# Optimization experiments

Measured on AMD Instinct MI355X. Metric: run time of the kernel, lower is better.

Reference implementation:

```python
import jax, jax.numpy as jnp
import numpy as np

NUM_EMBEDDINGS = 8192
EMBEDDING_DIM = 512
COMMITMENT_COST = 0.25
EMA_DECAY = 0.99
EPS = 1e-5


def setup_inputs() -> dict:
    key = jax.random.key(0)
    k1, k2, k3, k4 = jax.random.split(key, 4)
    B = 32768
    z = jax.random.normal(k1, (B, EMBEDDING_DIM), dtype=jnp.float32)
    weight = jax.random.normal(k2, (NUM_EMBEDDINGS, EMBEDDING_DIM), dtype=jnp.float32)
    ema_cluster_size = jax.random.uniform(k3, (NUM_EMBEDDINGS,), dtype=jnp.float32)
    ema_dw = jax.random.normal(k4, (NUM_EMBEDDINGS, EMBEDDING_DIM), dtype=jnp.float32)
    return {"z": z, "weight": weight, "ema_cluster_size": ema_cluster_size, "ema_dw": ema_dw}


def reference(z, weight, ema_cluster_size, ema_dw):
    K = weight.shape[0]
    # Squared-L2 distances: (B, K) = |z|^2 + |e|^2 - 2 z e^T
    distances = (
        jnp.sum(z * z, axis=1, keepdims=True)
        + jnp.sum(weight * weight, axis=1)
        - 2.0 * (z @ weight.T)
    )
    indices = jnp.argmin(distances, axis=1)          # (B,)
    quantized_raw = weight[indices]                  # (B, D) gather

    # EMA codebook update (training-mode buffers; one-hot scatter-add == segment_sum)
    counts = jax.ops.segment_sum(jnp.ones(z.shape[0], dtype=z.dtype), indices, num_segments=K)
    dw = jax.ops.segment_sum(z, indices, num_segments=K)  # encodings.T @ z
    new_cluster_size = ema_cluster_size * EMA_DECAY + (1.0 - EMA_DECAY) * counts
    new_ema_dw = ema_dw * EMA_DECAY + (1.0 - EMA_DECAY) * dw
    n = jnp.sum(new_cluster_size)
    cluster_size = (new_cluster_size + EPS) / (n + K * EPS) * n
    new_weight = new_ema_dw / cluster_size[:, None]

    commitment_loss = COMMITMENT_COST * jnp.mean((z - jax.lax.stop_gradient(quantized_raw)) ** 2)
    quantized = z + jax.lax.stop_gradient(quantized_raw - z)  # straight-through
    return quantized, indices, commitment_loss, new_weight, new_cluster_size, new_ema_dw
```

## Files before the change

kernel.cpp:

```cpp
#include <hip/hip_runtime.h>

#define B_N 32768
#define D_N 512
#define K_N 8192
#define EMA 0.99f
#define ONE_M_EMA 0.01f
#define EPS_ 1e-5f
#define CCOST 0.25f

#define ZP_OFF 295936ull
#define WP_OFF 67404800ull
#define WS_NEED (WP_OFF + 16777216ull)
#define CNT_OFF    295936ull
#define OFFS_OFF   332800ull
#define CURS_OFF   365568ull
#define ROWL_OFF   398336ull
#define LPART_OFF  529408ull

typedef __attribute__((ext_vector_type(8))) short bf16x8;
typedef __attribute__((ext_vector_type(4))) float f32x4;

__global__ __launch_bounds__(256) void prep_kernel(const float* __restrict__ w,
                                                   const float* __restrict__ ecs,
                                                   float* __restrict__ wsq,
                                                   float* __restrict__ ncs_out) {
  int row  = blockIdx.x * 4 + (threadIdx.x >> 6);
  int lane = threadIdx.x & 63;
  const float* p = w + (size_t)row * D_N + lane * 8;
  float4 a = *(const float4*)p;
  float4 b = *(const float4*)(p + 4);
  float s = a.x*a.x + a.y*a.y + a.z*a.z + a.w*a.w
          + b.x*b.x + b.y*b.y + b.z*b.z + b.w*b.w;
  #pragma unroll
  for (int off = 32; off; off >>= 1) s += __shfl_down(s, off);
  if (lane == 0) wsq[row] = s;

  int gid = blockIdx.x * 256 + threadIdx.x;
  if (gid < K_N) ncs_out[gid] = EMA * ecs[gid];
}

__global__ __launch_bounds__(256) void prep_nedw(const float4* __restrict__ edw,
                                                 float4* __restrict__ nedw) {
  int i = blockIdx.x * 256 + threadIdx.x;
  float4 v = edw[i];
  v.x *= EMA; v.y *= EMA; v.z *= EMA; v.w *= EMA;
  nedw[i] = v;
}

__global__ __launch_bounds__(256) void split_z(const float* __restrict__ x,
                                               ushort* __restrict__ xp) {
  int g   = blockIdx.x * 256 + threadIdx.x;
  int row = g >> 6, c = g & 63;
  const float* src = x + (size_t)row * 512 + c * 8;
  float v[8];
  *(float4*)&v[0] = *(const float4*)&src[0];
  *(float4*)&v[4] = *(const float4*)&src[4];
  uint hw[4], lw[4];
  #pragma unroll
  for (int i = 0; i < 4; i++) {
    uint b0 = __float_as_uint(v[2*i]);
    uint b1 = __float_as_uint(v[2*i+1]);
    float r0 = v[2*i]   - __uint_as_float(b0 & 0xFFFF0000u);
    float r1 = v[2*i+1] - __uint_as_float(b1 & 0xFFFF0000u);
    hw[i] = (b0 >> 16) | (b1 & 0xFFFF0000u);
    lw[i] = (__float_as_uint(r0) >> 16) | (__float_as_uint(r1) & 0xFFFF0000u);
  }
  int si  = c >> 2;
  int p   = (c & 3) ^ ((row >> 1) & 3);
  size_t sstr = (size_t)B_N * 32;
  size_t base = (size_t)row * 32 + (size_t)p * 8;
  *(uint4*)&xp[(size_t)si * sstr + base]        = (uint4){hw[0], hw[1], hw[2], hw[3]};
  *(uint4*)&xp[(size_t)(16 + si) * sstr + base] = (uint4){lw[0], lw[1], lw[2], lw[3]};
}

__global__ __launch_bounds__(256) void split_w(const float* __restrict__ x,
                                               ushort* __restrict__ xp,
                                               float* __restrict__ wsq) {
  int g   = blockIdx.x * 256 + threadIdx.x;
  int row = g >> 6, c = g & 63;
  const float* src = x + (size_t)row * 512 + c * 8;
  float v[8];
  *(float4*)&v[0] = *(const float4*)&src[0];
  *(float4*)&v[4] = *(const float4*)&src[4];
  uint hw[4], lw[4]; float w2 = 0.f;
  #pragma unroll
  for (int i = 0; i < 4; i++) {
    uint b0 = __float_as_uint(v[2*i]);
    uint b1 = __float_as_uint(v[2*i+1]);
    float r0 = v[2*i]   - __uint_as_float(b0 & 0xFFFF0000u);
    float r1 = v[2*i+1] - __uint_as_float(b1 & 0xFFFF0000u);
    hw[i] = (b0 >> 16) | (b1 & 0xFFFF0000u);
    lw[i] = (__float_as_uint(r0) >> 16) | (__float_as_uint(r1) & 0xFFFF0000u);
    w2 += v[2*i]*v[2*i] + v[2*i+1]*v[2*i+1];
  }
  int si  = c >> 2;
  int p   = (c & 3) ^ ((row >> 1) & 3);
  size_t sstr = (size_t)K_N * 32;
  size_t base = (size_t)row * 32 + (size_t)p * 8;
  *(uint4*)&xp[(size_t)si * sstr + base]        = (uint4){hw[0], hw[1], hw[2], hw[3]};
  *(uint4*)&xp[(size_t)(16 + si) * sstr + base] = (uint4){lw[0], lw[1], lw[2], lw[3]};
  #pragma unroll
  for (int off = 32; off; off >>= 1) w2 += __shfl_down(w2, off);
  if (c == 0) wsq[row] = w2;
}

constexpr int COLT2 = 8;

#define GLDS(SRC, DST) __builtin_amdgcn_global_load_lds((const unsigned int*)(SRC), (unsigned int*)(DST), 16, 0, 0)

#define STAGE4(SS)                                                             \
  {                                                                            \
    const int zsl_ = (sf < 32) ? (sf & 15) : (sf - 16);        \
    const int wsl_ = (sf < 32) ? sf : (sf - 32);               \
    GLDS(zA + (size_t)zsl_ * 2097152,        (char*)As[SS] + t * 16);          \
    GLDS(zA + (size_t)zsl_ * 2097152 + 4096, (char*)As[SS] + 4096 + t * 16);   \
    const size_t wOfs_ = (size_t)wsl_ * 524288 + (size_t)ctf * 16384;          \
    GLDS(wB + wOfs_,         (char*)Bs[SS] + t * 16);                          \
    GLDS(wB + wOfs_ + 4096,  (char*)Bs[SS] + 4096  + t * 16);                  \
    GLDS(wB + wOfs_ + 8192,  (char*)Bs[SS] + 8192  + t * 16);                  \
    GLDS(wB + wOfs_ + 12288, (char*)Bs[SS] + 12288 + t * 16);                  \
    sf++; if (sf == 48) { sf = 0; ctf++; }                                     \
  }

#define LOADFRAG4(AX, BX, RS)                                                  \
  {                                                                            \
    const char* Ab_ = (const char*)As[RS] + aoff;                              \
    const char* Bb_ = (const char*)Bs[RS] + boff;                              \
    _Pragma("unroll")                                                          \
    for (int i_ = 0; i_ < 8; i_++) AX[i_] = *(const bf16x8*)(Ab_ + i_ * 1024); \
    _Pragma("unroll")                                                          \
    for (int j_ = 0; j_ < 4; j_++) BX[j_] = *(const bf16x8*)(Bb_ + j_ * 1024); \
  }

#define MFMABLK4(AX, BX)                                                       \
  {                                                                            \
    __builtin_amdgcn_s_setprio(1);                                             \
    _Pragma("unroll")                                                          \
    for (int i_ = 0; i_ < 8; i_++)                                             \
      _Pragma("unroll")                                                        \
      for (int j_ = 0; j_ < 4; j_++)                                           \
        acc[i_][j_] = __builtin_amdgcn_mfma_f32_16x16x32_bf16(AX[i_], BX[j_],  \
                                                        acc[i_][j_], 0, 0, 0); \
    __builtin_amdgcn_s_setprio(0);                                             \
  }

#define PH4(AC, BC, AL, BL, RS, SS, G)                                         \
  {                                                                            \
    const int g_ = (G);                                                        \
    if (g_ + 1 <= 383) LOADFRAG4(AL, BL, RS)                                   \
    if (g_ + 2 <= 383) STAGE4(SS)                                              \
    MFMABLK4(AC, BC)                                                           \
    asm volatile("s_waitcnt lgkmcnt(0)" ::: "memory");                         \
    if (g_ <= 382) { asm volatile("s_waitcnt vmcnt(0)" ::: "memory"); }        \
    __builtin_amdgcn_s_barrier();                                              \
    __builtin_amdgcn_sched_barrier(0);                                         \
  }

__global__ __launch_bounds__(256, 2) void score4(
    const ushort* __restrict__ zp, const ushort* __restrict__ wp,
    const float* __restrict__ wsq, unsigned long long* __restrict__ packed) {
  __shared__ ushort As[2][4096];
  __shared__ ushort Bs[2][8192];
  __shared__ unsigned long long best2[128][4];

  const int t = threadIdx.x, lane = t & 63, wn = t >> 6;
  const int l15 = lane & 15, lg = (lane >> 4) & 3;
  const int row0 = blockIdx.x * 128;
  const int cg0  = blockIdx.y * 2048;

  const char* zA = (const char*)zp + ((size_t)(row0 + (t >> 2)) * 64 + (size_t)(t & 3) * 16);
  const char* wB = (const char*)wp + ((size_t)(cg0  + (t >> 2)) * 64 + (size_t)(t & 3) * 16);

  const int swz  = (l15 >> 1) & 3;
  const int aoff = l15 * 64 + ((lg ^ swz) * 16);
  const int boff = (wn * 64 + l15) * 64 + ((lg ^ swz) * 16);

  if (t < 128) { best2[t][0] = ~0ull; best2[t][1] = ~0ull; best2[t][2] = ~0ull; best2[t][3] = ~0ull; }
  __syncthreads();

  int sf = 0, ctf = 0;
  STAGE4(0)
  STAGE4(1)
  asm volatile("s_waitcnt vmcnt(0)" ::: "memory");
  __builtin_amdgcn_s_barrier();
  __builtin_amdgcn_sched_barrier(0);

  bf16x8 aE[8], bE[4], aO[8], bO[4];
  LOADFRAG4(aE, bE, 0)
  asm volatile("s_waitcnt lgkmcnt(0)" ::: "memory");
  __builtin_amdgcn_s_barrier();
  __builtin_amdgcn_sched_barrier(0);

  for (int ct = 0; ct < COLT2; ct++) {
    f32x4 acc[8][4];
    #pragma unroll
    for (int i = 0; i < 8; i++)
      #pragma unroll
      for (int j = 0; j < 4; j++) acc[i][j] = (f32x4){0.f, 0.f, 0.f, 0.f};

    for (int p = 0; p < 24; p++) {
      const int g = ct * 48 + 2 * p;
      PH4(aE, bE, aO, bO, 1, 0, g)
      PH4(aO, bO, aE, bE, 0, 1, g + 1)
    }

    float wq[4];
    #pragma unroll
    for (int j = 0; j < 4; j++) wq[j] = wsq[cg0 + ct * 256 + wn * 64 + j * 16 + l15];
    float rv[32]; int rx[32];
    #pragma unroll
    for (int i = 0; i < 8; i++)
      #pragma unroll
      for (int r = 0; r < 4; r++) {
        float bvv = 3.4e38f; int bii = 0;
        #pragma unroll
        for (int j = 0; j < 4; j++) {
          float dist = wq[j] - 2.0f * acc[i][j][r];
          int c = cg0 + ct * 256 + wn * 64 + j * 16 + l15;
          if (dist < bvv) { bvv = dist; bii = c; }
        }
        rv[i * 4 + r] = bvv; rx[i * 4 + r] = bii;
      }
    #pragma unroll
    for (int e = 0; e < 32; e++) {
      float v = rv[e]; int ix = rx[e];
      #pragma unroll
      for (int m = 1; m < 16; m <<= 1) {
        float ov = __shfl_xor(v, m, 64);
        int   oi = __shfl_xor(ix, m, 64);
        if (ov < v || (ov == v && oi < ix)) { v = ov; ix = oi; }
      }
      rv[e] = v; rx[e] = ix;
    }
    #pragma unroll
    for (int half = 0; half < 2; half++) {
      const int e0 = l15 + half * 16;
      float bvv = 0.f; int bii = 0;
      #pragma unroll
      for (int e = 0; e < 32; e++) {
        bool p2 = (e == e0);
        bvv = p2 ? rv[e] : bvv; bii = p2 ? rx[e] : bii;
      }
      unsigned u = __float_as_uint(bvv);
      u = (u & 0x80000000u) ? ~u : (u | 0x80000000u);
      unsigned long long key = ((unsigned long long)u << 32) | (unsigned)bii;
      const int rowl = (e0 >> 2) * 16 + lg * 4 + (e0 & 3);
      unsigned long long cur = best2[rowl][wn];
      if (key < cur) best2[rowl][wn] = key;
    }
  }

  __syncthreads();
  if (t < 128) {
    unsigned long long k0 = best2[t][0], k1 = best2[t][1];
    unsigned long long k2 = best2[t][2], k3 = best2[t][3];
    unsigned long long m0 = k0 < k1 ? k0 : k1;
    unsigned long long m1 = k2 < k3 ? k2 : k3;
    atomicMin(&packed[row0 + t], m0 < m1 ? m0 : m1);
  }
}

constexpr int LDP = 40;
constexpr int KSPLIT = 8, COLT = K_N / KSPLIT / 128;
__device__ __forceinline__ void stage16(const float* __restrict__ g,
                                        ushort* __restrict__ h,
                                        ushort* __restrict__ l) {
  float v[16];
  *(float4*)&v[0]  = *(const float4*)&g[0];
  *(float4*)&v[4]  = *(const float4*)&g[4];
  *(float4*)&v[8]  = *(const float4*)&g[8];
  *(float4*)&v[12] = *(const float4*)&g[12];
  uint hw[8], lw[8];
  #pragma unroll
  for (int i = 0; i < 8; i++) {
    uint b0 = __float_as_uint(v[2*i]);
    uint b1 = __float_as_uint(v[2*i+1]);
    float r0 = v[2*i]   - __uint_as_float(b0 & 0xFFFF0000u);
    float r1 = v[2*i+1] - __uint_as_float(b1 & 0xFFFF0000u);
    hw[i] = (b0 >> 16) | (b1 & 0xFFFF0000u);
    lw[i] = (__float_as_uint(r0) >> 16) | (__float_as_uint(r1) & 0xFFFF0000u);
  }
  ((uint4*)h)[0] = *(uint4*)&hw[0];
  ((uint4*)h)[1] = *(uint4*)&hw[4];
  ((uint4*)l)[0] = *(uint4*)&lw[0];
  ((uint4*)l)[1] = *(uint4*)&lw[4];
}

__global__ __launch_bounds__(256, 2) void score_argmin_mfma(
    const float* __restrict__ z, const float* __restrict__ w,
    const float* __restrict__ wsq, unsigned long long* __restrict__ packed) {
  __shared__ ushort Ah[128][LDP];
  __shared__ ushort Al[128][LDP];
  __shared__ ushort Bh[128][LDP];
  __shared__ ushort Bl[128][LDP];
  const int t = threadIdx.x, lane = t & 63, wid = t >> 6;
  const int wm = wid >> 1, wn = wid & 1;
  const int l15 = lane & 15, lg = lane >> 4;
  const int row0 = blockIdx.x * 128;
  const int ks0  = blockIdx.y * (K_N / KSPLIT);
  const int srow = t >> 1, skq = (t & 1) * 16;
  float rmin[16]; int ridx[16];
  #pragma unroll
  for (int e = 0; e < 16; e++) { rmin[e] = 3.4e38f; ridx[e] = 0; }
  for (int ct = 0; ct < COLT; ct++) {
    const int c0 = ks0 + ct * 128;
    f32x4 acc[4][4];
    #pragma unroll
    for (int i = 0; i < 4; i++)
      #pragma unroll
      for (int j = 0; j < 4; j++) acc[i][j] = (f32x4){0.f, 0.f, 0.f, 0.f};
    for (int k0 = 0; k0 < D_N; k0 += 32) {
      __syncthreads();
      stage16(&z[(size_t)(row0 + srow) * D_N + k0 + skq], &Ah[srow][skq], &Al[srow][skq]);
      stage16(&w[(size_t)(c0   + srow) * D_N + k0 + skq], &Bh[srow][skq], &Bl[srow][skq]);
      __syncthreads();
      bf16x8 ah[4], al[4], bh[4], bl[4];
      #pragma unroll
      for (int i = 0; i < 4; i++) {
        ah[i] = *(const bf16x8*)&Ah[wm*64 + i*16 + l15][lg*8];
        al[i] = *(const bf16x8*)&Al[wm*64 + i*16 + l15][lg*8];
        bh[i] = *(const bf16x8*)&Bh[wn*64 + i*16 + l15][lg*8];
        bl[i] = *(const bf16x8*)&Bl[wn*64 + i*16 + l15][lg*8];
      }
      #pragma unroll
      for (int i = 0; i < 4; i++)
        #pragma unroll
        for (int j = 0; j < 4; j++) {
          acc[i][j] = __builtin_amdgcn_mfma_f32_16x16x32_bf16(ah[i], bh[j], acc[i][j], 0, 0, 0);
          acc[i][j] = __builtin_amdgcn_mfma_f32_16x16x32_bf16(ah[i], bl[j], acc[i][j], 0, 0, 0);
          acc[i][j] = __builtin_amdgcn_mfma_f32_16x16x32_bf16(al[i], bh[j], acc[i][j], 0, 0, 0);
        }
    }
    float wq[4];
    #pragma unroll
    for (int j = 0; j < 4; j++) wq[j] = wsq[c0 + wn*64 + j*16 + l15];
    #pragma unroll
    for (int i = 0; i < 4; i++)
      #pragma unroll
      for (int r = 0; r < 4; r++) {
        const int e = i * 4 + r;
        #pragma unroll
        for (int j = 0; j < 4; j++) {
          float dist = wq[j] - 2.0f * acc[i][j][r];
          if (dist < rmin[e]) { rmin[e] = dist; ridx[e] = c0 + wn*64 + j*16 + l15; }
        }
      }
  }
  #pragma unroll
  for (int e = 0; e < 16; e++) {
    float v = rmin[e]; int ix = ridx[e];
    #pragma unroll
    for (int m = 1; m < 16; m <<= 1) {
      float ov = __shfl_xor(v, m, 64);
      int   oi = __shfl_xor(ix, m, 64);
      if (ov < v || (ov == v && oi < ix)) { v = ov; ix = oi; }
    }
    rmin[e] = v; ridx[e] = ix;
  }
  const int s = l15;
  float bv = 0.f; int bi = 0;
  #pragma unroll
  for (int e = 0; e < 16; e++) {
    bool p = (e == s);
    bv = p ? rmin[e] : bv;
    bi = p ? ridx[e] : bi;
  }
  unsigned u = __float_as_uint(bv);
  u = (u & 0x80000000u) ? ~u : (u | 0x80000000u);
  unsigned long long key = ((unsigned long long)u << 32) | (unsigned)bi;
  atomicMin(&packed[row0 + wm*64 + (s >> 2)*16 + lg*4 + (s & 3)], key);
}

__global__ __launch_bounds__(256) void count_kernel(
    const unsigned long long* __restrict__ packed, int* __restrict__ cnt,
    float* __restrict__ idxout) {
  int row = blockIdx.x * 256 + threadIdx.x;
  int idx = (int)(packed[row] & 0xFFFFFFFFull);
  idxout[row] = (float)idx;
  atomicAdd(&cnt[idx], 1);
}

__global__ __launch_bounds__(256) void scan_kernel(const int* __restrict__ cnt,
                                                   int* __restrict__ offs,
                                                   int* __restrict__ cursor) {
  int t = threadIdx.x;
  int base = t * 32;
  int local[32];
  int s = 0;
  #pragma unroll
  for (int i = 0; i < 32; i++) { local[i] = s; s += cnt[base + i]; }
  __shared__ int ps[257];
  ps[t + 1] = s;
  if (t == 0) ps[0] = 0;
  __syncthreads();
  if (t == 0) { for (int i = 1; i <= 256; i++) ps[i] += ps[i - 1]; }
  __syncthreads();
  int e = ps[t];
  #pragma unroll
  for (int i = 0; i < 32; i++) {
    int o = e + local[i];
    offs[base + i] = o; cursor[base + i] = o;
  }
  if (t == 255) offs[8192] = ps[256];
}

__global__ __launch_bounds__(256) void scatter_ids(
    const unsigned long long* __restrict__ packed, int* __restrict__ cursor,
    int* __restrict__ rowlist) {
  int row = blockIdx.x * 256 + threadIdx.x;
  int idx = (int)(packed[row] & 0xFFFFFFFFull);
  int pos = atomicAdd(&cursor[idx], 1);
  rowlist[pos] = row;
}

__global__ __launch_bounds__(256) void seg_accum(
    const float* __restrict__ z, const float* __restrict__ edw,
    const float* __restrict__ ecs, const int* __restrict__ offs,
    const int* __restrict__ rowlist, float* __restrict__ nedw_out,
    float* __restrict__ ncs_out) {
  int k = blockIdx.x, t = threadIdx.x;
  int s0 = offs[k], s1 = offs[k + 1];
  float ax = 0.f, ay = 0.f;
  for (int r = s0; r < s1; r++) {
    int row = rowlist[r];
    float2 zv = *(const float2*)&z[(size_t)row * D_N + t * 2];
    ax += zv.x; ay += zv.y;
  }
  float2 ev = *(const float2*)&edw[(size_t)k * D_N + t * 2];
  float2 o;
  o.x = EMA * ev.x + ONE_M_EMA * ax;
  o.y = EMA * ev.y + ONE_M_EMA * ay;
  *(float2*)&nedw_out[(size_t)k * D_N + t * 2] = o;
  if (t == 0) ncs_out[k] = EMA * ecs[k] + ONE_M_EMA * (float)(s1 - s0);
}

__global__ __launch_bounds__(256) void quant_loss(
    const float* __restrict__ z, const float* __restrict__ w,
    const unsigned long long* __restrict__ packed,
    float* __restrict__ qout, float* __restrict__ lpart) {
  int row = blockIdx.x, t = threadIdx.x;
  int idx = (int)(packed[row] & 0xFFFFFFFFull);
  float2 zv = *(const float2*)&z[(size_t)row * D_N + t * 2];
  float2 wv = *(const float2*)&w[(size_t)idx * D_N + t * 2];
  float2 q;
  q.x = zv.x + (wv.x - zv.x);
  q.y = zv.y + (wv.y - zv.y);
  *(float2*)&qout[(size_t)row * D_N + t * 2] = q;
  float dx = zv.x - wv.x, dy = zv.y - wv.y;
  float s = dx * dx + dy * dy;
  #pragma unroll
  for (int off = 32; off; off >>= 1) s += __shfl_down(s, off);
  __shared__ float part[4];
  if ((t & 63) == 0) part[t >> 6] = s;
  __syncthreads();
  if (t == 0) lpart[row] = part[0] + part[1] + part[2] + part[3];
}

__global__ __launch_bounds__(256) void reduce2(const float* __restrict__ ncs_out,
                                               const float* __restrict__ lpart,
                                               float* __restrict__ nsum,
                                               float* __restrict__ loss_sum) {
  int t = threadIdx.x;
  float s1 = 0.f, s2 = 0.f;
  for (int i = t; i < K_N; i += 256) s1 += ncs_out[i];
  for (int i = t; i < B_N; i += 256) s2 += lpart[i];
  #pragma unroll
  for (int off = 32; off; off >>= 1) {
    s1 += __shfl_down(s1, off);
    s2 += __shfl_down(s2, off);
  }
  __shared__ float p1[4], p2[4];
  if ((t & 63) == 0) { p1[t >> 6] = s1; p2[t >> 6] = s2; }
  __syncthreads();
  if (t == 0) {
    nsum[0]     = p1[0] + p1[1] + p1[2] + p1[3];
    loss_sum[0] = p2[0] + p2[1] + p2[2] + p2[3];
  }
}

__global__ __launch_bounds__(256) void gather_scatter(
    const float* __restrict__ z, const float* __restrict__ w,
    const unsigned long long* __restrict__ packed,
    float* __restrict__ qout, float* __restrict__ idxout,
    float* __restrict__ ncs_out, float* __restrict__ nedw_out,
    float* __restrict__ loss_sum) {
  int row = blockIdx.x;
  int t   = threadIdx.x;
  int idx = (int)(packed[row] & 0xFFFFFFFFull);
  float2 zv = *(const float2*)&z[(size_t)row * D_N + t * 2];
  float2 wv = *(const float2*)&w[(size_t)idx * D_N + t * 2];
  float2 q;
  q.x = zv.x + (wv.x - zv.x);
  q.y = zv.y + (wv.y - zv.y);
  *(float2*)&qout[(size_t)row * D_N + t * 2] = q;
  float dx = zv.x - wv.x, dy = zv.y - wv.y;
  float s = dx*dx + dy*dy;
  #pragma unroll
  for (int off = 32; off; off >>= 1) s += __shfl_down(s, off);
  __shared__ float part[4];
  if ((t & 63) == 0) part[t >> 6] = s;
  __syncthreads();
  if (t == 0) {
    atomicAdd(loss_sum, part[0] + part[1] + part[2] + part[3]);
    atomicAdd(&ncs_out[idx], ONE_M_EMA);
    idxout[row] = (float)idx;
  }
  atomicAdd(&nedw_out[(size_t)idx * D_N + t*2],     ONE_M_EMA * zv.x);
  atomicAdd(&nedw_out[(size_t)idx * D_N + t*2 + 1], ONE_M_EMA * zv.y);
}

__global__ __launch_bounds__(256) void reduce_n(const float* __restrict__ ncs_out,
                                                float* __restrict__ nsum) {
  int t = threadIdx.x;
  float s = 0.f;
  for (int i = t; i < K_N; i += 256) s += ncs_out[i];
  #pragma unroll
  for (int off = 32; off; off >>= 1) s += __shfl_down(s, off);
  __shared__ float part[4];
  if ((t & 63) == 0) part[t >> 6] = s;
  __syncthreads();
  if (t == 0) nsum[0] = part[0] + part[1] + part[2] + part[3];
}

__global__ __launch_bounds__(256) void finalize(
    const float* __restrict__ ncs_out, const float* __restrict__ nedw_out,
    float* __restrict__ nw_out, const float* __restrict__ nsum,
    const float* __restrict__ loss_sum, float* __restrict__ loss_out) {
  size_t i = (size_t)blockIdx.x * 256 + threadIdx.x;
  float n = nsum[0];
  int k = (int)(i >> 9);
  float nv = ncs_out[k];
  float cs = (nv + EPS_) / (n + K_N * EPS_) * n;
  nw_out[i] = nedw_out[i] / cs;
  if (i == 0) loss_out[0] = CCOST * loss_sum[0] / (float)((size_t)B_N * D_N);
}

extern "C" void kernel_launch(void* const* d_in, const int* in_sizes, int n_in,
                              void* d_out, int out_size, void* d_ws, size_t ws_size,
                              hipStream_t stream) {
  const float* z   = (const float*)d_in[0];
  const float* w   = (const float*)d_in[1];
  const float* ecs = (const float*)d_in[2];
  const float* edw = (const float*)d_in[3];

  float* out      = (float*)d_out;
  float* qout     = out;
  float* idxout   = out + (size_t)B_N * D_N;
  float* loss_out = idxout + B_N;
  float* nw_out   = loss_out + 1;
  float* ncs_out  = nw_out + (size_t)K_N * D_N;
  float* nedw_out = ncs_out + K_N;

  unsigned long long* packed = (unsigned long long*)d_ws;
  float* wsq      = (float*)((char*)d_ws + 262144);
  float* loss_sum = (float*)((char*)d_ws + 294912);
  float* nsum     = loss_sum + 1;

  hipMemsetAsync(d_ws, 0xFF, 262144, stream);
  hipMemsetAsync((void*)loss_sum, 0, 8, stream);

  if (ws_size >= WS_NEED) {
    ushort* zp  = (ushort*)((char*)d_ws + ZP_OFF);
    ushort* wp  = (ushort*)((char*)d_ws + WP_OFF);
    int* cnt    = (int*)((char*)d_ws + CNT_OFF);
    int* offs   = (int*)((char*)d_ws + OFFS_OFF);
    int* cursor = (int*)((char*)d_ws + CURS_OFF);
    int* rowl   = (int*)((char*)d_ws + ROWL_OFF);
    float* lpart= (float*)((char*)d_ws + LPART_OFF);

    split_z<<<8192, 256, 0, stream>>>(z, zp);
    split_w<<<2048, 256, 0, stream>>>(w, wp, wsq);
    score4<<<dim3(B_N / 128, 4), 256, 0, stream>>>(zp, wp, wsq, packed);
    hipMemsetAsync((void*)cnt, 0, K_N * sizeof(int), stream);
    count_kernel<<<B_N / 256, 256, 0, stream>>>(packed, cnt, idxout);
    scan_kernel<<<1, 256, 0, stream>>>(cnt, offs, cursor);
    scatter_ids<<<B_N / 256, 256, 0, stream>>>(packed, cursor, rowl);
    seg_accum<<<K_N, 256, 0, stream>>>(z, edw, ecs, offs, rowl, nedw_out, ncs_out);
    quant_loss<<<B_N, 256, 0, stream>>>(z, w, packed, qout, lpart);
    reduce2<<<1, 256, 0, stream>>>(ncs_out, lpart, nsum, loss_sum);
  } else {
    prep_kernel<<<2048, 256, 0, stream>>>(w, ecs, wsq, ncs_out);
    prep_nedw<<<4096, 256, 0, stream>>>((const float4*)edw, (float4*)nedw_out);
    score_argmin_mfma<<<dim3(B_N / 128, KSPLIT), 256, 0, stream>>>(z, w, wsq, packed);
    gather_scatter<<<B_N, 256, 0, stream>>>(z, w, packed, qout, idxout,
                                            ncs_out, nedw_out, loss_sum);
    reduce_n<<<1, 256, 0, stream>>>(ncs_out, nsum);
  }

  finalize<<<K_N * D_N / 256, 256, 0, stream>>>(ncs_out, nedw_out, nw_out,
                                                nsum, loss_sum, loss_out);
}
```

Measured before the change: 1.051 ms.

## Rewrite distance GEMM as single-wave blocks with barrier-free vmcnt pipelining

The scoring GEMM moves from 256-thread blocks on a 128x256 tile to single-wavefront blocks on a 64x128 tile. With one wave per block, all s_barrier calls go away, and the double-buffer sync relies on partial vmcnt waits. The running argmin now stays in registers across column tiles, and the cross-lane reduction and atomicMin run once at the end instead of per tile through LDS. The cost is lower data reuse per block (smaller tile, more global/L2 traffic) and only one wave per block to hide latency, which relies on occupancy from many small blocks.

```diff
diff --git a/kernel.cpp b/kernel.cpp
--- a/kernel.cpp
+++ b/kernel.cpp
@@ -104,160 +104,146 @@
   if (c == 0) wsq[row] = w2;
 }
 
-constexpr int COLT2 = 8;
+constexpr int CT5 = 16;
+constexpr int NS5 = CT5 * 48;
 
 #define GLDS(SRC, DST) __builtin_amdgcn_global_load_lds((const unsigned int*)(SRC), (unsigned int*)(DST), 16, 0, 0)
 
-#define STAGE4(SS)                                                             \
+#define STAGE5(SL)                                                             \
   {                                                                            \
     const int zsl_ = (sf < 32) ? (sf & 15) : (sf - 16);        \
     const int wsl_ = (sf < 32) ? sf : (sf - 32);               \
-    GLDS(zA + (size_t)zsl_ * 2097152,        (char*)As[SS] + t * 16);          \
-    GLDS(zA + (size_t)zsl_ * 2097152 + 4096, (char*)As[SS] + 4096 + t * 16);   \
-    const size_t wOfs_ = (size_t)wsl_ * 524288 + (size_t)ctf * 16384;          \
-    GLDS(wB + wOfs_,         (char*)Bs[SS] + t * 16);                          \
-    GLDS(wB + wOfs_ + 4096,  (char*)Bs[SS] + 4096  + t * 16);                  \
-    GLDS(wB + wOfs_ + 8192,  (char*)Bs[SS] + 8192  + t * 16);                  \
-    GLDS(wB + wOfs_ + 12288, (char*)Bs[SS] + 12288 + t * 16);                  \
+    const char* za_ = zA + (size_t)zsl_ * 2097152;                             \
+    _Pragma("unroll")                                                          \
+    for (int o_ = 0; o_ < 4; o_++)                                             \
+      GLDS(za_ + o_ * 1024, (char*)As[SL] + o_ * 1024);                        \
+    const char* wb_ = wB + (size_t)wsl_ * 524288 + (size_t)ctf * 8192;         \
+    _Pragma("unroll")                                                          \
+    for (int o_ = 0; o_ < 8; o_++)                                             \
+      GLDS(wb_ + o_ * 1024, (char*)Bs[SL] + o_ * 1024);                        \
     sf++; if (sf == 48) { sf = 0; ctf++; }                                     \
   }
 
-#define LOADFRAG4(AX, BX, RS)                                                  \
+#define LOADFRAG5(AX, BX, RS)                                                  \
   {                                                                            \
     const char* Ab_ = (const char*)As[RS] + aoff;                              \
     const char* Bb_ = (const char*)Bs[RS] + boff;                              \
     _Pragma("unroll")                                                          \
-    for (int i_ = 0; i_ < 8; i_++) AX[i_] = *(const bf16x8*)(Ab_ + i_ * 1024); \
+    for (int i_ = 0; i_ < 4; i_++) AX[i_] = *(const bf16x8*)(Ab_ + i_ * 1024); \
     _Pragma("unroll")                                                          \
-    for (int j_ = 0; j_ < 4; j_++) BX[j_] = *(const bf16x8*)(Bb_ + j_ * 1024); \
-  }
-
-#define MFMABLK4(AX, BX)                                                       \
+    for (int j_ = 0; j_ < 8; j_++) BX[j_] = *(const bf16x8*)(Bb_ + j_ * 1024); \
+  }
+
+#define MFMABLK5(AX, BX)                                                       \
   {                                                                            \
     __builtin_amdgcn_s_setprio(1);                                             \
     _Pragma("unroll")                                                          \
-    for (int i_ = 0; i_ < 8; i_++)                                             \
+    for (int i_ = 0; i_ < 4; i_++)                                             \
       _Pragma("unroll")                                                        \
-      for (int j_ = 0; j_ < 4; j_++)                                           \
+      for (int j_ = 0; j_ < 8; j_++)                                           \
         acc[i_][j_] = __builtin_amdgcn_mfma_f32_16x16x32_bf16(AX[i_], BX[j_],  \
                                                         acc[i_][j_], 0, 0, 0); \
     __builtin_amdgcn_s_setprio(0);                                             \
   }
 
-#define PH4(AC, BC, AL, BL, RS, SS, G)                                         \
+#define PH5(AC, BC, AL, BL, G)                                                 \
   {                                                                            \
     const int g_ = (G);                                                        \
-    if (g_ + 1 <= 383) LOADFRAG4(AL, BL, RS)                                   \
-    if (g_ + 2 <= 383) STAGE4(SS)                                              \
-    MFMABLK4(AC, BC)                                                           \
+    if (g_ + 2 < NS5) STAGE5(g_ & 1)                                           \
+    if (g_ + 1 < NS5) {                                                        \
+      if (g_ + 2 < NS5) { asm volatile("s_waitcnt vmcnt(12)" ::: "memory"); }  \
+      else              { asm volatile("s_waitcnt vmcnt(0)"  ::: "memory"); }  \
+      LOADFRAG5(AL, BL, (g_ + 1) & 1)                                          \
+    }                                                                          \
+    MFMABLK5(AC, BC)                                                           \
     asm volatile("s_waitcnt lgkmcnt(0)" ::: "memory");                         \
-    if (g_ <= 382) { asm volatile("s_waitcnt vmcnt(0)" ::: "memory"); }        \
-    __builtin_amdgcn_s_barrier();                                              \
     __builtin_amdgcn_sched_barrier(0);                                         \
   }
 
-__global__ __launch_bounds__(256, 2) void score4(
+__global__ __launch_bounds__(64, 2) void score5(
     const ushort* __restrict__ zp, const ushort* __restrict__ wp,
     const float* __restrict__ wsq, unsigned long long* __restrict__ packed) {
-  __shared__ ushort As[2][4096];
-  __shared__ ushort Bs[2][8192];
-  __shared__ unsigned long long best2[128][4];
-
-  const int t = threadIdx.x, lane = t & 63, wn = t >> 6;
+  __shared__ ushort As[2][2048];
+  __shared__ ushort Bs[2][4096];
+
+  const int lane = threadIdx.x;
   const int l15 = lane & 15, lg = (lane >> 4) & 3;
-  const int row0 = blockIdx.x * 128;
+  const int row0 = blockIdx.x * 64;
   const int cg0  = blockIdx.y * 2048;
 
-  const char* zA = (const char*)zp + ((size_t)(row0 + (t >> 2)) * 64 + (size_t)(t & 3) * 16);
-  const char* wB = (const char*)wp + ((size_t)(cg0  + (t >> 2)) * 64 + (size_t)(t & 3) * 16);
+  const char* zA = (const char*)zp + ((size_t)(row0 + (lane >> 2)) * 64 + (size_t)(lane & 3) * 16);
+  const char* wB = (const char*)wp + ((size_t)(cg0  + (lane >> 2)) * 64 + (size_t)(lane & 3) * 16);
 
   const int swz  = (l15 >> 1) & 3;
   const int aoff = l15 * 64 + ((lg ^ swz) * 16);
-  const int boff = (wn * 64 + l15) * 64 + ((lg ^ swz) * 16);
-
-  if (t < 128) { best2[t][0] = ~0ull; best2[t][1] = ~0ull; best2[t][2] = ~0ull; best2[t][3] = ~0ull; }
-  __syncthreads();
+  const int boff = l15 * 64 + ((lg ^ swz) * 16);
+
+  float rmin[16]; int ridx[16];
+  #pragma unroll
+  for (int e = 0; e < 16; e++) { rmin[e] = 3.4e38f; ridx[e] = 0; }
 
   int sf = 0, ctf = 0;
-  STAGE4(0)
-  STAGE4(1)
-  asm volatile("s_waitcnt vmcnt(0)" ::: "memory");
-  __builtin_amdgcn_s_barrier();
+  STAGE5(0)
+  STAGE5(1)
+  asm volatile("s_waitcnt vmcnt(12)" ::: "memory");
+  bf16x8 aE[4], bE[8], aO[4], bO[8];
+  LOADFRAG5(aE, bE, 0)
+  asm volatile("s_waitcnt lgkmcnt(0)" ::: "memory");
   __builtin_amdgcn_sched_barrier(0);
 
-  bf16x8 aE[8], bE[4], aO[8], bO[4];
-  LOADFRAG4(aE, bE, 0)
-  asm volatile("s_waitcnt lgkmcnt(0)" ::: "memory");
-  __builtin_amdgcn_s_barrier();
-  __builtin_amdgcn_sched_barrier(0);
-
-  for (int ct = 0; ct < COLT2; ct++) {
-    f32x4 acc[8][4];
-    #pragma unroll
-    for (int i = 0; i < 8; i++)
+  for (int ct = 0; ct < CT5; ct++) {
+    f32x4 acc[4][8];
+    #pragma unroll
+    for (int i = 0; i < 4; i++)
       #pragma unroll
-      for (int j = 0; j < 4; j++) acc[i][j] = (f32x4){0.f, 0.f, 0.f, 0.f};
+      for (int j = 0; j < 8; j++) acc[i][j] = (f32x4){0.f, 0.f, 0.f, 0.f};
 
     for (int p = 0; p < 24; p++) {
       const int g = ct * 48 + 2 * p;
-      PH4(aE, bE, aO, bO, 1, 0, g)
-      PH4(aO, bO, aE, bE, 0, 1, g + 1)
+      PH5(aE, bE, aO, bO, g)
+      PH5(aO, bO, aE, bE, g + 1)
     }
 
-    float wq[4];
-    #pragma unroll
-    for (int j = 0; j < 4; j++) wq[j] = wsq[cg0 + ct * 256 + wn * 64 + j * 16 + l15];
-    float rv[32]; int rx[32];
-    #pragma unroll
-    for (int i = 0; i < 8; i++)
+    float wq[8];
+    #pragma unroll
+    for (int j = 0; j < 8; j++) wq[j] = wsq[cg0 + ct * 128 + j * 16 + l15];
+    #pragma unroll
+    for (int i = 0; i < 4; i++)
       #pragma unroll
       for (int r = 0; r < 4; r++) {
-        float bvv = 3.4e38f; int bii = 0;
+        const int e = i * 4 + r;
         #pragma unroll
-        for (int j = 0; j < 4; j++) {
+        for (int j = 0; j < 8; j++) {
           float dist = wq[j] - 2.0f * acc[i][j][r];
-          int c = cg0 + ct * 256 + wn * 64 + j * 16 + l15;
-          if (dist < bvv) { bvv = dist; bii = c; }
+          int c = cg0 + ct * 128 + j * 16 + l15;
+          if (dist < rmin[e]) { rmin[e] = dist; ridx[e] = c; }
         }
-        rv[i * 4 + r] = bvv; rx[i * 4 + r] = bii;
       }
-    #pragma unroll
-    for (int e = 0; e < 32; e++) {
-      float v = rv[e]; int ix = rx[e];
-      #pragma unroll
-      for (int m = 1; m < 16; m <<= 1) {
-        float ov = __shfl_xor(v, m, 64);
-        int   oi = __shfl_xor(ix, m, 64);
-        if (ov < v || (ov == v && oi < ix)) { v = ov; ix = oi; }
-      }
-      rv[e] = v; rx[e] = ix;
+  }
+
+  #pragma unroll
+  for (int e = 0; e < 16; e++) {
+    float v = rmin[e]; int ix = ridx[e];
+    #pragma unroll
+    for (int m = 1; m < 16; m <<= 1) {
+      float ov = __shfl_xor(v, m, 64);
+      int   oi = __shfl_xor(ix, m, 64);
+      if (ov < v || (ov == v && oi < ix)) { v = ov; ix = oi; }
     }
-    #pragma unroll
-    for (int half = 0; half < 2; half++) {
-      const int e0 = l15 + half * 16;
-      float bvv = 0.f; int bii = 0;
-      #pragma unroll
-      for (int e = 0; e < 32; e++) {
-        bool p2 = (e == e0);
-        bvv = p2 ? rv[e] : bvv; bii = p2 ? rx[e] : bii;
-      }
-      unsigned u = __float_as_uint(bvv);
-      u = (u & 0x80000000u) ? ~u : (u | 0x80000000u);
-      unsigned long long key = ((unsigned long long)u << 32) | (unsigned)bii;
-      const int rowl = (e0 >> 2) * 16 + lg * 4 + (e0 & 3);
-      unsigned long long cur = best2[rowl][wn];
-      if (key < cur) best2[rowl][wn] = key;
-    }
-  }
-
-  __syncthreads();
-  if (t < 128) {
-    unsigned long long k0 = best2[t][0], k1 = best2[t][1];
-    unsigned long long k2 = best2[t][2], k3 = best2[t][3];
-    unsigned long long m0 = k0 < k1 ? k0 : k1;
-    unsigned long long m1 = k2 < k3 ? k2 : k3;
-    atomicMin(&packed[row0 + t], m0 < m1 ? m0 : m1);
-  }
+    rmin[e] = v; ridx[e] = ix;
+  }
+  const int s = l15;
+  float bv = 0.f; int bi = 0;
+  #pragma unroll
+  for (int e = 0; e < 16; e++) {
+    bool p = (e == s);
+    bv = p ? rmin[e] : bv;
+    bi = p ? ridx[e] : bi;
+  }
+  unsigned u = __float_as_uint(bv);
+  u = (u & 0x80000000u) ? ~u : (u | 0x80000000u);
+  unsigned long long key = ((unsigned long long)u << 32) | (unsigned)bi;
+  atomicMin(&packed[row0 + (s >> 2) * 16 + lg * 4 + (s & 3)], key);
 }
 
 constexpr int LDP = 40;
@@ -570,7 +556,7 @@
 
     split_z<<<8192, 256, 0, stream>>>(z, zp);
     split_w<<<2048, 256, 0, stream>>>(w, wp, wsq);
-    score4<<<dim3(B_N / 128, 4), 256, 0, stream>>>(zp, wp, wsq, packed);
+    score5<<<dim3(B_N / 64, 4), 64, 0, stream>>>(zp, wp, wsq, packed);
     hipMemsetAsync((void*)cnt, 0, K_N * sizeof(int), stream);
     count_kernel<<<B_N / 256, 256, 0, stream>>>(packed, cnt, idxout);
     scan_kernel<<<1, 256, 0, stream>>>(cnt, offs, cursor);
```

After: 1.418 ms. +35.0%, slower.
